# Kernel tuning notes

Hardware: AMD Instinct MI355X
Metric: run time of the kernel (lower is better)

Reference implementation:

```python
import jax, jax.numpy as jnp
import numpy as np

B, D, H, O, RH, P = 8192, 784, 2048, 1024, 128, 64
NI = NJ = NK = 4  # input regions / hidden groups / output groups


def _make_groups():
    idx = np.arange(28 * 28).reshape(28, 28)
    input_groups = np.stack([
        idx[:14, :14].ravel(), idx[:14, 14:].ravel(),
        idx[14:, :14].ravel(), idx[14:, 14:].ravel(),
    ]).astype(np.int32)                                   # [4, 196]
    hidden_groups = np.arange(H, dtype=np.int32).reshape(NJ, H // NJ)   # [4, 512]
    output_groups = np.arange(O, dtype=np.int32).reshape(NK, O // NK)   # [4, 256]
    return input_groups, hidden_groups, output_groups


def setup_inputs() -> dict:
    key = jax.random.key(0)
    ks = jax.random.split(key, 9)
    ig, hg, og = _make_groups()
    inp = {
        "x":   jax.random.normal(ks[0], (B, D), jnp.float32),
        "W1":  jax.random.normal(ks[1], (H, D), jnp.float32) / np.sqrt(D),
        "b1":  jax.random.normal(ks[2], (H,), jnp.float32) * 0.01,
        "W2":  jax.random.normal(ks[3], (O, H), jnp.float32) / np.sqrt(H),
        "b2":  jax.random.normal(ks[4], (O,), jnp.float32) * 0.01,
        "Wr1": jax.random.normal(ks[5], (RH, D), jnp.float32) / np.sqrt(D),
        "br1": jax.random.normal(ks[6], (RH,), jnp.float32) * 0.01,
        "Wr2": jax.random.normal(ks[7], (P, RH), jnp.float32) / np.sqrt(RH),
        "br2": jax.random.normal(ks[8], (P,), jnp.float32) * 0.01,
        "input_groups": jnp.asarray(ig),
        "hidden_groups": jnp.asarray(hg),
        "output_groups": jnp.asarray(og),
        "top_k": 8,
    }
    return inp


def reference(x, W1, b1, W2, b2, Wr1, br1, Wr2, br2,
              input_groups, hidden_groups, output_groups, top_k):
    # --- router MLP (eval mode: dropout = identity, no routing noise) ---
    h_r = jax.nn.relu(x @ Wr1.T + br1)
    scores = h_r @ Wr2.T + br2                      # [B, P]
    probs = jax.nn.softmax(scores, axis=-1)         # temperature = 1.0

    # --- top-k pathway selection + renormalization ---
    top_vals, top_idx = jax.lax.top_k(probs, top_k)
    bsz = x.shape[0]
    mask = jnp.zeros_like(probs).at[jnp.arange(bsz)[:, None], top_idx].set(top_vals)
    wts = mask / (mask.sum(axis=-1, keepdims=True) + 1e-8)
    wts4 = wts.reshape(bsz, NI, NJ, NK)             # pathway_idx = i*16 + j*4 + k

    # --- gather pathway sub-blocks ---
    x_reg = x[:, input_groups]                      # [B, I, 196]
    # W1g[i, j] = W1[hidden_groups[j]][:, input_groups[i]] -> [I, J, 512, 196]
    W1g = W1[hidden_groups[None, :, :, None], input_groups[:, None, None, :]]
    b1g = b1[hidden_groups]                         # [J, 512]
    # W2g[j, k] = W2[output_groups[k]][:, hidden_groups[j]] -> [J, K, 256, 512]
    W2g = W2[output_groups[None, :, :, None], hidden_groups[:, None, None, :]]
    b2g = b2[output_groups]                         # [K, 256]

    # --- pathway computation (exact erf GELU, as torch F.gelu default) ---
    hidden = jax.nn.gelu(
        jnp.einsum('bin,ijhn->ijbh', x_reg, W1g) + b1g[None, :, None, :],
        approximate=False)                          # [I, J, B, 512]
    # weighted pathway outputs, contracted over i, j, h without materializing
    # the full [I, J, K, B, 256] tensor
    out_main = jnp.einsum('ijbh,jkoh,bijk->bko', hidden, W2g, wts4)  # [B, K, 256]
    wsum = wts4.sum(axis=(1, 2))                    # [B, K] (bias weighted per pathway)
    out_blocks = out_main + wsum[:, :, None] * b2g[None]

    out = jnp.zeros((bsz, O), x.dtype).at[:, output_groups].add(out_blocks)
    return out
```

## Files before the change

### kernel.cpp

```cpp
#include <hip/hip_runtime.h>
#include <hip/hip_bf16.h>
#include <hip/hip_fp16.h>

#define B_  8192
#define D_  784
#define H_  2048
#define O_  1024
#define RH_ 128
#define P_  64
#define KP  224
#define KC  196

typedef __attribute__((ext_vector_type(8))) short short8;
typedef __attribute__((ext_vector_type(4))) float f32x4;

__device__ inline float bf2f(unsigned short u) {
  union { unsigned int i; float f; } v; v.i = ((unsigned int)u) << 16; return v.f;
}
__device__ inline unsigned short f2bf(float f) {
  __hip_bfloat16 h = __float2bfloat16(f);
  return *reinterpret_cast<unsigned short*>(&h);
}
__device__ inline unsigned short f2h(float f) {
  __half h = __float2half(f);
  return *reinterpret_cast<unsigned short*>(&h);
}
__device__ inline float h2f(unsigned short u) {
  __half h = *reinterpret_cast<__half*>(&u);
  return __half2float(h);
}
__device__ inline float erf_fast(float x) {
  float ax = fabsf(x);
  float t = 1.0f / (1.0f + 0.3275911f * ax);
  float p = ((((1.061405429f * t - 1.453152027f) * t + 1.421413741f) * t
              - 0.284496736f) * t + 0.254829592f) * t;
  float y = 1.0f - p * __expf(-ax * ax);
  return x < 0.f ? -y : y;
}
__device__ inline float gelu_exact(float v) {
  return 0.5f * v * (1.0f + erf_fast(v * 0.70710678118654752f));
}

__device__ inline void gload_lds16(const void* g, void* l) {
  __builtin_amdgcn_global_load_lds((const __attribute__((address_space(1))) void*)g,
                                   (__attribute__((address_space(3))) void*)l, 16, 0, 0);
}

__device__ inline void gemm128_db(const unsigned short* gA0, const unsigned short* gA1,
                                  const unsigned short* gB0, const unsigned short* gB1,
                                  int K, char* lds, f32x4 acc[4][4]) {
  const int t = threadIdx.x;
  const int w = t >> 6, l = t & 63;
  const int wr = (w >> 1) * 64, wc = (w & 1) * 64;
  const int lr = l & 15;
  const int swr = (lr >> 1) & 3;
  const int arow = (wr + lr) * 64 + (((l >> 4) ^ swr) * 16);
  const int brow = 8192 + (wc + lr) * 64 + (((l >> 4) ^ swr) * 16);
  const int tOff = t * 16;
  {
    char* d = lds + tOff;
    gload_lds16(gA0, d);
    gload_lds16(gA1, d + 4096);
    gload_lds16(gB0, d + 8192);
    gload_lds16(gB1, d + 12288);
  }
  __syncthreads();
  int cur = 0;
  for (int kt = 0; kt < K; kt += 32) {
    const int nxt = kt + 32;
    if (nxt < K) {
      char* d = lds + ((cur ^ 1) << 14) + tOff;
      gload_lds16(gA0 + nxt, d);
      gload_lds16(gA1 + nxt, d + 4096);
      gload_lds16(gB0 + nxt, d + 8192);
      gload_lds16(gB1 + nxt, d + 12288);
    }
    __builtin_amdgcn_sched_barrier(0);
    const char* buf = lds + (cur << 14);
    short8 af[4], bfr[4];
#pragma unroll
    for (int f = 0; f < 4; ++f) {
      af[f]  = *(const short8*)(buf + arow + f * 1024);
      bfr[f] = *(const short8*)(buf + brow + f * 1024);
    }
#pragma unroll
    for (int fm = 0; fm < 4; ++fm)
#pragma unroll
      for (int fn = 0; fn < 4; ++fn)
        acc[fm][fn] = __builtin_amdgcn_mfma_f32_16x16x32_bf16(af[fm], bfr[fn], acc[fm][fn], 0, 0, 0);
    __syncthreads();
    cur ^= 1;
  }
}

__device__ inline void gemm128_bt(const unsigned short* __restrict__ A,
                                  const unsigned short* __restrict__ Bm,
                                  int K, char* lds, f32x4 acc[4][4]) {
  const int t = threadIdx.x;
  const int s_orig = (t & 3) ^ ((t >> 3) & 3);
  const size_t srcOff = (size_t)(t >> 2) * K + s_orig * 8;
  gemm128_db(A + srcOff, A + srcOff + (size_t)64 * K,
             Bm + srcOff, Bm + srcOff + (size_t)64 * K, K, lds, acc);
}

__global__ void k_prep(const float* __restrict__ x, const float* __restrict__ W1,
                       const float* __restrict__ W2, const int* __restrict__ ig,
                       unsigned short* __restrict__ xreg, unsigned short* __restrict__ w1g,
                       unsigned short* __restrict__ w2b) {
  const size_t N1 = (size_t)4 * B_ * KP;
  const size_t N2 = (size_t)4 * H_ * KP;
  const size_t N3 = (size_t)O_ * H_;
  const size_t TOT = N1 + N2 + N3;
  for (size_t idx = (size_t)blockIdx.x * blockDim.x + threadIdx.x; idx < TOT;
       idx += (size_t)gridDim.x * blockDim.x) {
    if (idx < N1) {
      int n = (int)(idx % KP); size_t r = idx / KP;
      int b = (int)(r % B_); int i = (int)(r / B_);
      float v = (n < 196) ? x[(size_t)b * D_ + ig[i * 196 + n]] : 0.f;
      xreg[idx] = f2bf(v);
    } else if (idx < N1 + N2) {
      size_t q = idx - N1;
      int n = (int)(q % KP); size_t r = q / KP;
      int h = (int)(r % H_); int i = (int)(r / H_);
      float v = (n < 196) ? W1[(size_t)h * D_ + ig[i * 196 + n]] : 0.f;
      w1g[q] = f2bf(v);
    } else {
      size_t q = idx - N1 - N2;
      w2b[q] = f2bf(W2[q]);
    }
  }
}

__global__ __launch_bounds__(256) void k_r1s(const float* __restrict__ x,
    const float* __restrict__ Wr1, const float* __restrict__ br1,
    float* __restrict__ hrp) {
  __shared__ float As[64][33];
  __shared__ float Bs[64][33];
  const int b0 = blockIdx.x * 64;
  const int h0 = blockIdx.y * 64;
  const int kb = blockIdx.z * KC;
  const int kend = kb + KC;
  const int t = threadIdx.x;
  const int srow = t >> 2;
  const int scol = (t & 3) * 8;
  const int ty = t >> 4, tx = t & 15;
  float acc[4][4];
#pragma unroll
  for (int i = 0; i < 4; ++i)
#pragma unroll
    for (int j = 0; j < 4; ++j) acc[i][j] = 0.f;
  const float* gA = x   + (size_t)(b0 + srow) * D_;
  const float* gB = Wr1 + (size_t)(h0 + srow) * D_;
  for (int k0 = kb; k0 < kend; k0 += 32) {
    float4 a0 = (k0 + scol + 4  <= kend) ? *(const float4*)(gA + k0 + scol)     : float4{0,0,0,0};
    float4 a1 = (k0 + scol + 8  <= kend) ? *(const float4*)(gA + k0 + scol + 4) : float4{0,0,0,0};
    float4 w0 = (k0 + scol + 4  <= kend) ? *(const float4*)(gB + k0 + scol)     : float4{0,0,0,0};
    float4 w1 = (k0 + scol + 8  <= kend) ? *(const float4*)(gB + k0 + scol + 4) : float4{0,0,0,0};
    __syncthreads();
    *(float4*)&As[srow][scol]     = a0;
    *(float4*)&As[srow][scol + 4] = a1;
    *(float4*)&Bs[srow][scol]     = w0;
    *(float4*)&Bs[srow][scol + 4] = w1;
    __syncthreads();
#pragma unroll
    for (int kk = 0; kk < 8; ++kk) {
      float4 a4[4], b4[4];
#pragma unroll
      for (int i = 0; i < 4; ++i) a4[i] = *(const float4*)&As[ty * 4 + i][kk * 4];
#pragma unroll
      for (int j = 0; j < 4; ++j) b4[j] = *(const float4*)&Bs[tx * 4 + j][kk * 4];
#pragma unroll
      for (int i = 0; i < 4; ++i)
#pragma unroll
        for (int j = 0; j < 4; ++j)
          acc[i][j] += a4[i].x * b4[j].x + a4[i].y * b4[j].y +
                       a4[i].z * b4[j].z + a4[i].w * b4[j].w;
    }
  }
  float* hz = hrp + (size_t)blockIdx.z * B_ * RH_;
#pragma unroll
  for (int j = 0; j < 4; ++j) {
    const int h = h0 + tx * 4 + j;
    const float bias = (blockIdx.z == 0) ? br1[h] : 0.f;
#pragma unroll
    for (int i = 0; i < 4; ++i)
      hz[(size_t)(b0 + ty * 4 + i) * RH_ + h] = acc[i][j] + bias;
  }
}

#define R2S 32
__global__ __launch_bounds__(256) void k_r2(const float* __restrict__ hrp,
    const float* __restrict__ Wr2, const float* __restrict__ br2,
    float* __restrict__ wts, float* __restrict__ wsum,
    unsigned long long* __restrict__ actmask) {
  __shared__ float Ws[64][130];
  __shared__ float hs[R2S][128];
  const int s0 = blockIdx.x * R2S;
  const int t = threadIdx.x;
  for (int idx = t; idx < 2048; idx += 256) {
    int r = idx >> 5, c = (idx & 31) * 4;
    *(float4*)&Ws[r][c] = *(const float4*)(Wr2 + (size_t)r * RH_ + c);
  }
  for (int idx = t; idx < R2S * 32; idx += 256) {
    int r = idx >> 5, c = (idx & 31) * 4;
    const size_t off = (size_t)(s0 + r) * RH_ + c;
    float4 p0 = *(const float4*)(hrp + off);
    float4 p1 = *(const float4*)(hrp + (size_t)1 * B_ * RH_ + off);
    float4 p2 = *(const float4*)(hrp + (size_t)2 * B_ * RH_ + off);
    float4 p3 = *(const float4*)(hrp + (size_t)3 * B_ * RH_ + off);
    float4 s;
    s.x = fmaxf(p0.x + p1.x + p2.x + p3.x, 0.f);
    s.y = fmaxf(p0.y + p1.y + p2.y + p3.y, 0.f);
    s.z = fmaxf(p0.z + p1.z + p2.z + p3.z, 0.f);
    s.w = fmaxf(p0.w + p1.w + p2.w + p3.w, 0.f);
    *(float4*)&hs[r][c] = s;
  }
  __syncthreads();
  const int w = t >> 6, p = t & 63;
  const float wb2 = br2[p];
  for (int si = 0; si < R2S / 4; ++si) {
    const int sl = w * (R2S / 4) + si;
    float sc = wb2;
#pragma unroll
    for (int kk = 0; kk < 32; ++kk) {
      float4 h4 = *(const float4*)&hs[sl][kk * 4];
      float4 w4 = *(const float4*)&Ws[p][kk * 4];
      sc += h4.x * w4.x + h4.y * w4.y + h4.z * w4.z + h4.w * w4.w;
    }
    float m = sc;
#pragma unroll
    for (int o = 32; o; o >>= 1) m = fmaxf(m, __shfl_xor(m, o));
    float e = __expf(sc - m);
    float Z = e;
#pragma unroll
    for (int o = 32; o; o >>= 1) Z += __shfl_xor(Z, o);
    bool sel = false;
    float ssum = 0.f;
    for (int it = 0; it < 8; ++it) {
      float v = sel ? -1.f : e;
      float vm = v;
#pragma unroll
      for (int o = 32; o; o >>= 1) vm = fmaxf(vm, __shfl_xor(vm, o));
      unsigned long long mask = __ballot(!sel && v == vm);
      int first = __ffsll((long long)mask) - 1;
      if (p == first) sel = true;
      ssum += vm;
    }
    const float dn = 1.0f / (ssum + 1e-8f * Z);
    const float wv = sel ? e * dn : 0.f;
    wts[(size_t)(s0 + sl) * 64 + p] = wv;
    const unsigned long long am = __ballot(sel);
    if (p == 0) actmask[s0 + sl] = am;
    float part = wv;
#pragma unroll
    for (int o = 4; o < 64; o <<= 1) part += __shfl_xor(part, o);
    if (p < 4) wsum[(size_t)(s0 + sl) * 4 + p] = part;
  }
}

__global__ __launch_bounds__(256) void k_compact(const unsigned long long* __restrict__ actmask,
                                                 int* __restrict__ lists,
                                                 int* __restrict__ counts) {
  __shared__ int wcnt[4];
  __shared__ int sbase;
  const int ij = blockIdx.x;
  const int shift = (ij >> 2) * 16 + (ij & 3) * 4;
  const int t = threadIdx.x;
  const int wid = t >> 6, lane = t & 63;
  unsigned long long mk[32];
#pragma unroll
  for (int c = 0; c < 32; ++c) mk[c] = actmask[c * 256 + t];
  if (t == 0) sbase = 0;
  __syncthreads();
  for (int c = 0; c < 32; ++c) {
    const int b = c * 256 + t;
    const bool act = ((mk[c] >> shift) & 0xFULL) != 0ULL;
    const unsigned long long m = __ballot(act);
    if (lane == 0) wcnt[wid] = __popcll(m);
    __syncthreads();
    int off = sbase;
    const int tot = wcnt[0] + wcnt[1] + wcnt[2] + wcnt[3];
    for (int q = 0; q < wid; ++q) off += wcnt[q];
    if (act)
      lists[ij * B_ + off + __popcll(m & ((1ULL << lane) - 1ULL))] = b;
    __syncthreads();
    if (t == 0) sbase += tot;
  }
  __syncthreads();
  if (t == 0) counts[ij] = sbase;
}

__global__ __launch_bounds__(256) void k_l1g(const unsigned short* __restrict__ xreg,
    const unsigned short* __restrict__ w1g, const float* __restrict__ b1,
    const int* __restrict__ lists, const int* __restrict__ counts,
    unsigned short* __restrict__ hid16) {
  const int mt = blockIdx.x, nt = blockIdx.y, iq = blockIdx.z;
  const int ij = iq * 4 + (nt >> 2);
  const int count = counts[ij];
  if (mt * 128 >= count) return;
  __shared__ __align__(128) char lds[32768];
  __shared__ int rows[128];
  const int t = threadIdx.x;
  const int* list = lists + (size_t)ij * B_;
  if (t < 128) {
    int rl = mt * 128 + t;
    rows[t] = list[rl < count ? rl : count - 1];
  }
  __syncthreads();
  const int s_orig = (t & 3) ^ ((t >> 3) & 3);
  const int scol = s_orig * 8;
  const int r0 = rows[t >> 2], r1 = rows[(t >> 2) + 64];
  const unsigned short* gA0 = xreg + ((size_t)iq * B_ + r0) * KP + scol;
  const unsigned short* gA1 = xreg + ((size_t)iq * B_ + r1) * KP + scol;
  const unsigned short* gB0 = w1g + ((size_t)(iq * H_ + nt * 128) + (t >> 2)) * KP + scol;
  const unsigned short* gB1 = gB0 + (size_t)64 * KP;
  f32x4 acc[4][4];
#pragma unroll
  for (int a = 0; a < 4; ++a)
#pragma unroll
    for (int b = 0; b < 4; ++b) acc[a][b] = (f32x4){0.f, 0.f, 0.f, 0.f};
  gemm128_db(gA0, gA1, gB0, gB1, KP, lds, acc);
  const int w = t >> 6, l = t & 63;
  const int rloc0 = (w >> 1) * 64 + (l >> 4) * 4;
  const int cloc = (w & 1) * 64 + (l & 15);
  unsigned short* lt = (unsigned short*)lds;
#pragma unroll
  for (int fn = 0; fn < 4; ++fn) {
    const int col = cloc + fn * 16;
    const float bias = b1[nt * 128 + col];
#pragma unroll
    for (int fm = 0; fm < 4; ++fm)
#pragma unroll
      for (int r = 0; r < 4; ++r) {
        const int row = rloc0 + fm * 16 + r;
        const int gsw = (col >> 3) ^ (row & 7);
        lt[row * 128 + gsw * 8 + (col & 7)] = f2h(acc[fm][fn][r] + bias);
      }
  }
  __syncthreads();
  const int mlim = count - mt * 128;
  const int row = t >> 1, half = t & 1;
  if (row < mlim) {
    unsigned short* dst = hid16 + ((size_t)iq * B_ + rows[row]) * H_ + nt * 128 + half * 64;
#pragma unroll
    for (int q = 0; q < 8; ++q) {
      const int g = (half * 8 + q) ^ (row & 7);
      *(short8*)(dst + q * 8) = *(const short8*)(lt + row * 128 + g * 8);
    }
  }
}

__global__ __launch_bounds__(256) void k_combine(unsigned short* __restrict__ hid,
                                                 const float* __restrict__ wts) {
  const int b = blockIdx.x;
  const int n = threadIdx.x * 8;
  const int j = n >> 9;
  const float* wb = wts + (size_t)b * 64 + j * 4;
  float acc[4][8];
#pragma unroll
  for (int k = 0; k < 4; ++k)
#pragma unroll
    for (int e = 0; e < 8; ++e) acc[k][e] = 0.f;
#pragma unroll
  for (int i = 0; i < 4; ++i) {
    const float4 w4 = *(const float4*)(wb + i * 16);
    if (w4.x != 0.f || w4.y != 0.f || w4.z != 0.f || w4.w != 0.f) {
      short8 raw = *(const short8*)(hid + ((size_t)i * B_ + b) * H_ + n);
#pragma unroll
      for (int e = 0; e < 8; ++e) {
        float g = gelu_exact(h2f((unsigned short)raw[e]));
        acc[0][e] += g * w4.x;
        acc[1][e] += g * w4.y;
        acc[2][e] += g * w4.z;
        acc[3][e] += g * w4.w;
      }
    }
  }
#pragma unroll
  for (int k = 0; k < 4; ++k) {
    short8 outv;
#pragma unroll
    for (int e = 0; e < 8; ++e) outv[e] = (short)f2bf(acc[k][e]);
    *(short8*)(hid + ((size_t)k * B_ + b) * H_ + n) = outv;
  }
}

__global__ __launch_bounds__(256) void k_l2(const unsigned short* __restrict__ G,
    const unsigned short* __restrict__ w2b, const float* __restrict__ b2,
    const float* __restrict__ wsum, float* __restrict__ out) {
  __shared__ __align__(128) char lds[32768];
  const int mt = blockIdx.x, nt = blockIdx.y, k = blockIdx.z;
  const unsigned short* A  = G + ((size_t)k * B_ + mt * 128) * H_;
  const unsigned short* Bm = w2b + ((size_t)(k * 256 + nt * 128)) * H_;
  f32x4 acc[4][4];
#pragma unroll
  for (int a = 0; a < 4; ++a)
#pragma unroll
    for (int b = 0; b < 4; ++b) acc[a][b] = (f32x4){0.f, 0.f, 0.f, 0.f};
  gemm128_bt(A, Bm, H_, lds, acc);
  const int t = threadIdx.x, w = t >> 6, l = t & 63;
  const int rbase = mt * 128 + (w >> 1) * 64 + (l >> 4) * 4;
  const int cb = nt * 128 + (w & 1) * 64 + (l & 15);
#pragma unroll
  for (int fn = 0; fn < 4; ++fn) {
    const int ncol = k * 256 + cb + fn * 16;
    const float bias = b2[ncol];
#pragma unroll
    for (int fm = 0; fm < 4; ++fm)
#pragma unroll
      for (int r = 0; r < 4; ++r) {
        const int m = rbase + fm * 16 + r;
        out[(size_t)m * O_ + ncol] = acc[fm][fn][r] + wsum[m * 4 + k] * bias;
      }
  }
}

extern "C" void kernel_launch(void* const* d_in, const int* in_sizes, int n_in,
                              void* d_out, int out_size, void* d_ws, size_t ws_size,
                              hipStream_t stream) {
  const float* x   = (const float*)d_in[0];
  const float* W1  = (const float*)d_in[1];
  const float* b1  = (const float*)d_in[2];
  const float* W2  = (const float*)d_in[3];
  const float* b2  = (const float*)d_in[4];
  const float* Wr1 = (const float*)d_in[5];
  const float* br1 = (const float*)d_in[6];
  const float* Wr2 = (const float*)d_in[7];
  const float* br2 = (const float*)d_in[8];
  const int*   ig  = (const int*)d_in[9];
  float* out = (float*)d_out;
  char* ws = (char*)d_ws;
  unsigned short* xreg = (unsigned short*)(ws);
  unsigned short* w1g  = (unsigned short*)(ws + 14680064);
  unsigned short* w2b  = (unsigned short*)(ws + 18350080);
  float*          wts  = (float*)(ws + 22544384);
  float*          wsum = (float*)(ws + 24641536);
  unsigned short* hid  = (unsigned short*)(ws + 24772608);
  float*          hrp  = (float*)(ws + 24772608);
  int*                lists   = (int*)d_out;
  int*                counts  = lists + 16 * B_;
  unsigned long long* actmask = (unsigned long long*)((char*)d_out + 524352);

  k_prep<<<dim3(2048), dim3(256), 0, stream>>>(x, W1, W2, ig, xreg, w1g, w2b);
  k_r1s<<<dim3(B_ / 64, RH_ / 64, 4), dim3(256), 0, stream>>>(x, Wr1, br1, hrp);
  k_r2<<<dim3(B_ / R2S), dim3(256), 0, stream>>>(hrp, Wr2, br2, wts, wsum, actmask);
  k_compact<<<dim3(16), dim3(256), 0, stream>>>(actmask, lists, counts);
  k_l1g<<<dim3(B_ / 128, H_ / 128, 4), dim3(256), 0, stream>>>(xreg, w1g, b1, lists, counts, hid);
  k_combine<<<dim3(B_), dim3(256), 0, stream>>>(hid, wts);
  k_l2<<<dim3(B_ / 128, 2, 4), dim3(256), 0, stream>>>(hid, w2b, b2, wsum, out);
}
```

Before: 240.3 us.

## Use BK=64 double-buffered MFMA tiles in layer-2 GEMM and prefetch router loads

The layer-2 GEMM now stages two 32-wide K chunks per pipeline step, using 64KB of LDS, so it runs half as many barrier-separated iterations over K=2048. The fp32 router GEMM now issues the next tile's global loads right after the LDS stores, letting them overlap the FMA loop. The larger LDS footprint can lower occupancy in k_l2. The router prefetch also keeps extra registers live.

```diff
diff --git a/kernel.cpp b/kernel.cpp
--- a/kernel.cpp
+++ b/kernel.cpp
@@ -93,14 +93,64 @@
   }
 }
 
-__device__ inline void gemm128_bt(const unsigned short* __restrict__ A,
-                                  const unsigned short* __restrict__ Bm,
-                                  int K, char* lds, f32x4 acc[4][4]) {
+__device__ inline void gemm128_db64(const unsigned short* gA0, const unsigned short* gA1,
+                                    const unsigned short* gB0, const unsigned short* gB1,
+                                    int K, char* lds, f32x4 acc[4][4]) {
+  const int t = threadIdx.x;
+  const int w = t >> 6, l = t & 63;
+  const int wr = (w >> 1) * 64, wc = (w & 1) * 64;
+  const int lr = l & 15;
+  const int swr = (lr >> 1) & 3;
+  const int arow = (wr + lr) * 64 + (((l >> 4) ^ swr) * 16);
+  const int brow = 8192 + (wc + lr) * 64 + (((l >> 4) ^ swr) * 16);
+  const int tOff = t * 16;
+#define STAGE64(bufbase, ksrc) { \
+    char* d = lds + (bufbase) + tOff; \
+    gload_lds16(gA0 + (ksrc), d); \
+    gload_lds16(gA1 + (ksrc), d + 4096); \
+    gload_lds16(gB0 + (ksrc), d + 8192); \
+    gload_lds16(gB1 + (ksrc), d + 12288); \
+    gload_lds16(gA0 + (ksrc) + 32, d + 16384); \
+    gload_lds16(gA1 + (ksrc) + 32, d + 16384 + 4096); \
+    gload_lds16(gB0 + (ksrc) + 32, d + 16384 + 8192); \
+    gload_lds16(gB1 + (ksrc) + 32, d + 16384 + 12288); \
+  }
+  STAGE64(0, 0);
+  __syncthreads();
+  int cur = 0;
+  for (int kt = 0; kt < K; kt += 64) {
+    if (kt + 64 < K) STAGE64((cur ^ 1) << 15, kt + 64);
+    __builtin_amdgcn_sched_barrier(0);
+    const char* buf = lds + (cur << 15);
+#pragma unroll
+    for (int c = 0; c < 2; ++c) {
+      const char* ch = buf + c * 16384;
+      short8 af[4], bfr[4];
+#pragma unroll
+      for (int f = 0; f < 4; ++f) {
+        af[f]  = *(const short8*)(ch + arow + f * 1024);
+        bfr[f] = *(const short8*)(ch + brow + f * 1024);
+      }
+#pragma unroll
+      for (int fm = 0; fm < 4; ++fm)
+#pragma unroll
+        for (int fn = 0; fn < 4; ++fn)
+          acc[fm][fn] = __builtin_amdgcn_mfma_f32_16x16x32_bf16(af[fm], bfr[fn], acc[fm][fn], 0, 0, 0);
+    }
+    __syncthreads();
+    cur ^= 1;
+  }
+#undef STAGE64
+}
+
+__device__ inline void gemm128_bt64(const unsigned short* __restrict__ A,
+                                    const unsigned short* __restrict__ Bm,
+                                    int K, char* lds, f32x4 acc[4][4]) {
   const int t = threadIdx.x;
   const int s_orig = (t & 3) ^ ((t >> 3) & 3);
   const size_t srcOff = (size_t)(t >> 2) * K + s_orig * 8;
-  gemm128_db(A + srcOff, A + srcOff + (size_t)64 * K,
-             Bm + srcOff, Bm + srcOff + (size_t)64 * K, K, lds, acc);
+  gemm128_db64(A + srcOff, A + srcOff + (size_t)64 * K,
+               Bm + srcOff, Bm + srcOff + (size_t)64 * K, K, lds, acc);
 }
 
 __global__ void k_prep(const float* __restrict__ x, const float* __restrict__ W1,
@@ -151,17 +201,25 @@
     for (int j = 0; j < 4; ++j) acc[i][j] = 0.f;
   const float* gA = x   + (size_t)(b0 + srow) * D_;
   const float* gB = Wr1 + (size_t)(h0 + srow) * D_;
+  float4 a0 = *(const float4*)(gA + kb + scol);
+  float4 a1 = *(const float4*)(gA + kb + scol + 4);
+  float4 w0 = *(const float4*)(gB + kb + scol);
+  float4 w1 = *(const float4*)(gB + kb + scol + 4);
   for (int k0 = kb; k0 < kend; k0 += 32) {
-    float4 a0 = (k0 + scol + 4  <= kend) ? *(const float4*)(gA + k0 + scol)     : float4{0,0,0,0};
-    float4 a1 = (k0 + scol + 8  <= kend) ? *(const float4*)(gA + k0 + scol + 4) : float4{0,0,0,0};
-    float4 w0 = (k0 + scol + 4  <= kend) ? *(const float4*)(gB + k0 + scol)     : float4{0,0,0,0};
-    float4 w1 = (k0 + scol + 8  <= kend) ? *(const float4*)(gB + k0 + scol + 4) : float4{0,0,0,0};
     __syncthreads();
     *(float4*)&As[srow][scol]     = a0;
     *(float4*)&As[srow][scol + 4] = a1;
     *(float4*)&Bs[srow][scol]     = w0;
     *(float4*)&Bs[srow][scol + 4] = w1;
     __syncthreads();
+    const int kn = k0 + 32;
+    if (kn < kend) {
+      a0 = (kn + scol + 4 <= kend) ? *(const float4*)(gA + kn + scol)     : float4{0,0,0,0};
+      a1 = (kn + scol + 8 <= kend) ? *(const float4*)(gA + kn + scol + 4) : float4{0,0,0,0};
+      w0 = (kn + scol + 4 <= kend) ? *(const float4*)(gB + kn + scol)     : float4{0,0,0,0};
+      w1 = (kn + scol + 8 <= kend) ? *(const float4*)(gB + kn + scol + 4) : float4{0,0,0,0};
+    }
+    __builtin_amdgcn_sched_barrier(0);
 #pragma unroll
     for (int kk = 0; kk < 8; ++kk) {
       float4 a4[4], b4[4];
@@ -388,7 +446,7 @@
 __global__ __launch_bounds__(256) void k_l2(const unsigned short* __restrict__ G,
     const unsigned short* __restrict__ w2b, const float* __restrict__ b2,
     const float* __restrict__ wsum, float* __restrict__ out) {
-  __shared__ __align__(128) char lds[32768];
+  __shared__ __align__(128) char lds[65536];
   const int mt = blockIdx.x, nt = blockIdx.y, k = blockIdx.z;
   const unsigned short* A  = G + ((size_t)k * B_ + mt * 128) * H_;
   const unsigned short* Bm = w2b + ((size_t)(k * 256 + nt * 128)) * H_;
@@ -397,7 +455,7 @@
   for (int a = 0; a < 4; ++a)
 #pragma unroll
     for (int b = 0; b < 4; ++b) acc[a][b] = (f32x4){0.f, 0.f, 0.f, 0.f};
-  gemm128_bt(A, Bm, H_, lds, acc);
+  gemm128_bt64(A, Bm, H_, lds, acc);
   const int t = threadIdx.x, w = t >> 6, l = t & 63;
   const int rbase = mt * 128 + (w >> 1) * 64 + (l >> 4) * 4;
   const int cb = nt * 128 + (w & 1) * 64 + (l & 15);
```

Result: faster. 234.8 us (-2.3%).
